# Performance work log

Hardware: AMD Instinct MI355X
Metric: run time of the kernel (lower is better)

Reference implementation:

```python
import jax, jax.numpy as jnp
import numpy as np

N_BASE = 15
SAME_IDS = [[0, 1, 2], [3, 4], [5], [6, 7, 8, 9], [10, 11], [12, 13, 14]]
MEAN_STD = 1.0  # self.mean_std


def setup_inputs() -> dict:
    key = jax.random.key(0)
    batch, channels = 512, 4096
    meta1 = jax.random.normal(key, (batch * N_BASE, channels), dtype=jnp.float32)
    return {"meta1": meta1}


def reference(meta1):
    batch = meta1.shape[0] // N_BASE
    C = meta1.shape[1]
    # [batch, n_base, C] -> [n_base, batch, C]
    m = meta1.reshape(batch, N_BASE, C).transpose(1, 0, 2)
    meta1_mean = m.mean(axis=1)                      # [n_base, C]
    # Original indexes these via .data -> detached; mirror with stop_gradient.
    sub_mean = jax.lax.stop_gradient(meta1_mean.mean(axis=1))          # [n_base]
    sub_std = jax.lax.stop_gradient(jnp.std(meta1_mean, axis=1, ddof=1))  # [n_base], torch std unbiased

    ss_list, mean_list, mean_sum_list = [], [], []
    for line in SAME_IDS:
        idx = jnp.asarray(line)
        g_std = sub_std[idx]
        g_mean = sub_mean[idx]
        if len(line) == 1:
            ss_list.append(g_std[0])          # std_std
            mean_sum_list.append(g_mean[0])   # mean_sum
            mean_list.append(g_mean[0])       # mean
        else:
            ss_list.append(jnp.std(g_std, ddof=1))
            mean_sum_list.append(jnp.std(g_mean, ddof=1))
            mean_list.append(jnp.mean(g_mean))
    ss = jnp.stack(ss_list)        # [G]
    mean = jnp.stack(mean_list)    # [G]
    mean_sum = jnp.stack(mean_sum_list)  # [G]

    G = len(SAME_IDS)
    # subloss[i] = 5e-5 + sum_{j>i} exp((ss_i-ss_j)^2) + mean_std*exp((mean_i-mean_j)^2)
    tri = jnp.triu(jnp.ones((G, G), dtype=bool), k=1)
    pair = jnp.exp((ss[:, None] - ss[None, :]) ** 2) + MEAN_STD * jnp.exp((mean[:, None] - mean[None, :]) ** 2)
    subloss = jnp.float32(5e-5) + jnp.sum(jnp.where(tri, pair, 0.0), axis=1)
    loss = jnp.sum(jnp.log(1.0 + mean_sum / (subloss + mean_sum)))
    return loss
```

## Files before the change

### kernel.cpp

```cpp
#include <hip/hip_runtime.h>

#define NBASE 15
#define CDIM  4096
#define BATCH 512
#define NP    16
#define BPC   (BATCH/NP)

__device__ float  g_partial[NP][NBASE][CDIM];
__device__ double g_stats[2][NBASE];

__global__ __launch_bounds__(256) void k1_partial(const float4* __restrict__ in) {
    const int id = blockIdx.x;
    const int p  = id & 15;
    const int cc = (id >> 4) & 3;
    const int n  = id >> 6;
    const int c4 = cc * 256 + threadIdx.x;
    const int row_f4 = CDIM / 4;

    float4 acc = make_float4(0.f, 0.f, 0.f, 0.f);
    const int b0 = p * BPC;
    #pragma unroll 4
    for (int i = 0; i < BPC; ++i) {
        const int row = (b0 + i) * NBASE + n;
        float4 v = in[(size_t)row * row_f4 + c4];
        acc.x += v.x; acc.y += v.y; acc.z += v.z; acc.w += v.w;
    }
    float4* out4 = reinterpret_cast<float4*>(&g_partial[p][n][0]);
    out4[c4] = acc;
}

__global__ __launch_bounds__(256) void k2_stats() {
    const int n = blockIdx.x;
    double sm = 0.0, sm2 = 0.0;
    for (int c = threadIdx.x; c < CDIM; c += 256) {
        float s = 0.f;
        #pragma unroll
        for (int p = 0; p < NP; ++p) s += g_partial[p][n][c];
        const double m = (double)s * (1.0 / BATCH);
        sm += m; sm2 += m * m;
    }
    __shared__ double red0[256];
    __shared__ double red1[256];
    red0[threadIdx.x] = sm; red1[threadIdx.x] = sm2;
    __syncthreads();
    for (int off = 128; off > 0; off >>= 1) {
        if ((int)threadIdx.x < off) {
            red0[threadIdx.x] += red0[threadIdx.x + off];
            red1[threadIdx.x] += red1[threadIdx.x + off];
        }
        __syncthreads();
    }
    if (threadIdx.x == 0) {
        const double S = red0[0], S2 = red1[0];
        const double mean = S / CDIM;
        const double var  = (S2 - S * S / CDIM) / (CDIM - 1);
        g_stats[0][n] = mean;
        g_stats[1][n] = sqrt(var);
    }
}

__global__ void k3_loss(float* __restrict__ out) {
    if (threadIdx.x != 0 || blockIdx.x != 0) return;
    const int G = 6;
    const int off[G] = {0, 3, 5, 6, 10, 12};
    const int len[G] = {3, 2, 1, 4, 2, 3};
    double ss[G], mn[G], ms[G];
    for (int g = 0; g < G; ++g) {
        const int o = off[g], L = len[g];
        if (L == 1) {
            ss[g] = g_stats[1][o];
            mn[g] = g_stats[0][o];
            ms[g] = g_stats[0][o];
        } else {
            double sm = 0.0, st = 0.0;
            for (int k = 0; k < L; ++k) { sm += g_stats[0][o + k]; st += g_stats[1][o + k]; }
            sm /= L; st /= L;
            double vm = 0.0, vs = 0.0;
            for (int k = 0; k < L; ++k) {
                const double dm = g_stats[0][o + k] - sm; vm += dm * dm;
                const double ds = g_stats[1][o + k] - st; vs += ds * ds;
            }
            mn[g] = sm;
            ms[g] = sqrt(vm / (L - 1));
            ss[g] = sqrt(vs / (L - 1));
        }
    }
    double loss = 0.0;
    for (int i = 0; i < G; ++i) {
        double sl = 5e-5;
        for (int j = i + 1; j < G; ++j) {
            const double ds = ss[i] - ss[j];
            const double dm = mn[i] - mn[j];
            sl += exp(ds * ds) + exp(dm * dm);
        }
        loss += log(1.0 + ms[i] / (sl + ms[i]));
    }
    out[0] = (float)loss;
}

extern "C" void kernel_launch(void* const* d_in, const int* in_sizes, int n_in,
                              void* d_out, int out_size, void* d_ws, size_t ws_size,
                              hipStream_t stream) {
    const float4* in = (const float4*)d_in[0];
    float* out = (float*)d_out;
    hipLaunchKernelGGL(k1_partial, dim3(NBASE * 4 * NP), dim3(256), 0, stream, in);
    hipLaunchKernelGGL(k2_stats,   dim3(NBASE),          dim3(256), 0, stream);
    hipLaunchKernelGGL(k3_loss,    dim3(1),              dim3(64),  0, stream, out);
}
```

Measured before the change: 191.0 us.

## Double batch split, parallelize stats reduction across channel chunks and loss threads

Splits the batch into 32 partial chunks instead of 16, which doubles the k1 grid and fully unrolls its loads. The stats kernel now runs 60 blocks over channel quarters, reading float4 partials, and writes partial sums that the loss kernel combines. The loss kernel spreads the group and pair computations across threads with shared memory. The goal is more parallelism in the memory-bound first stage and in the serial tail kernels, at the cost of a larger partial buffer.

```diff
diff --git a/kernel.cpp b/kernel.cpp
--- a/kernel.cpp
+++ b/kernel.cpp
@@ -2,43 +2,52 @@
 
 #define NBASE 15
 #define CDIM  4096
+#define C4    (CDIM/4)
 #define BATCH 512
-#define NP    16
+#define NP    32
 #define BPC   (BATCH/NP)
 
-__device__ float  g_partial[NP][NBASE][CDIM];
-__device__ double g_stats[2][NBASE];
+__device__ float4 g_partial4[NP][NBASE][C4];
+__device__ double g_red[NBASE][4][2];
+
+__device__ __constant__ int c_pi[15] = {0,0,0,0,0,1,1,1,1,2,2,2,3,3,4};
+__device__ __constant__ int c_pj[15] = {1,2,3,4,5,2,3,4,5,3,4,5,4,5,5};
 
 __global__ __launch_bounds__(256) void k1_partial(const float4* __restrict__ in) {
     const int id = blockIdx.x;
-    const int p  = id & 15;
-    const int cc = (id >> 4) & 3;
-    const int n  = id >> 6;
+    const int p  = id & 31;
+    const int cc = (id >> 5) & 3;
+    const int n  = id >> 7;
     const int c4 = cc * 256 + threadIdx.x;
-    const int row_f4 = CDIM / 4;
 
     float4 acc = make_float4(0.f, 0.f, 0.f, 0.f);
     const int b0 = p * BPC;
-    #pragma unroll 4
+    #pragma unroll
     for (int i = 0; i < BPC; ++i) {
         const int row = (b0 + i) * NBASE + n;
-        float4 v = in[(size_t)row * row_f4 + c4];
+        float4 v = in[(size_t)row * C4 + c4];
         acc.x += v.x; acc.y += v.y; acc.z += v.z; acc.w += v.w;
     }
-    float4* out4 = reinterpret_cast<float4*>(&g_partial[p][n][0]);
-    out4[c4] = acc;
+    g_partial4[p][n][c4] = acc;
 }
 
 __global__ __launch_bounds__(256) void k2_stats() {
-    const int n = blockIdx.x;
-    double sm = 0.0, sm2 = 0.0;
-    for (int c = threadIdx.x; c < CDIM; c += 256) {
-        float s = 0.f;
-        #pragma unroll
-        for (int p = 0; p < NP; ++p) s += g_partial[p][n][c];
-        const double m = (double)s * (1.0 / BATCH);
-        sm += m; sm2 += m * m;
+    const int n  = blockIdx.x >> 2;
+    const int cc = blockIdx.x & 3;
+    const int c4 = cc * 256 + threadIdx.x;
+
+    float4 s = make_float4(0.f, 0.f, 0.f, 0.f);
+    #pragma unroll
+    for (int p = 0; p < NP; ++p) {
+        float4 v = g_partial4[p][n][c4];
+        s.x += v.x; s.y += v.y; s.z += v.z; s.w += v.w;
     }
+    const double inv = 1.0 / BATCH;
+    const double m0 = (double)s.x * inv, m1 = (double)s.y * inv;
+    const double m2 = (double)s.z * inv, m3 = (double)s.w * inv;
+    double sm  = m0 + m1 + m2 + m3;
+    double sm2 = m0*m0 + m1*m1 + m2*m2 + m3*m3;
+
     __shared__ double red0[256];
     __shared__ double red1[256];
     red0[threadIdx.x] = sm; red1[threadIdx.x] = sm2;
@@ -51,51 +60,72 @@
         __syncthreads();
     }
     if (threadIdx.x == 0) {
-        const double S = red0[0], S2 = red1[0];
-        const double mean = S / CDIM;
-        const double var  = (S2 - S * S / CDIM) / (CDIM - 1);
-        g_stats[0][n] = mean;
-        g_stats[1][n] = sqrt(var);
+        g_red[n][cc][0] = red0[0];
+        g_red[n][cc][1] = red1[0];
     }
 }
 
-__global__ void k3_loss(float* __restrict__ out) {
-    if (threadIdx.x != 0 || blockIdx.x != 0) return;
-    const int G = 6;
-    const int off[G] = {0, 3, 5, 6, 10, 12};
-    const int len[G] = {3, 2, 1, 4, 2, 3};
-    double ss[G], mn[G], ms[G];
-    for (int g = 0; g < G; ++g) {
-        const int o = off[g], L = len[g];
+__global__ __launch_bounds__(64) void k3_loss(float* __restrict__ out) {
+    __shared__ double sub_mean[NBASE], sub_std[NBASE];
+    __shared__ double mn[6], ms[6], ssg[6];
+    __shared__ double pairv[15];
+    __shared__ double terms[6];
+    const int t = threadIdx.x;
+
+    if (t < NBASE) {
+        double S = 0.0, S2 = 0.0;
+        #pragma unroll
+        for (int cc = 0; cc < 4; ++cc) { S += g_red[t][cc][0]; S2 += g_red[t][cc][1]; }
+        sub_mean[t] = S / CDIM;
+        sub_std[t]  = sqrt((S2 - S * S / CDIM) / (CDIM - 1));
+    }
+    __syncthreads();
+
+    if (t < 6) {
+        const int off[6] = {0, 3, 5, 6, 10, 12};
+        const int len[6] = {3, 2, 1, 4, 2, 3};
+        const int o = off[t], L = len[t];
         if (L == 1) {
-            ss[g] = g_stats[1][o];
-            mn[g] = g_stats[0][o];
-            ms[g] = g_stats[0][o];
+            ssg[t] = sub_std[o];
+            mn[t]  = sub_mean[o];
+            ms[t]  = sub_mean[o];
         } else {
             double sm = 0.0, st = 0.0;
-            for (int k = 0; k < L; ++k) { sm += g_stats[0][o + k]; st += g_stats[1][o + k]; }
+            for (int k = 0; k < L; ++k) { sm += sub_mean[o + k]; st += sub_std[o + k]; }
             sm /= L; st /= L;
             double vm = 0.0, vs = 0.0;
             for (int k = 0; k < L; ++k) {
-                const double dm = g_stats[0][o + k] - sm; vm += dm * dm;
-                const double ds = g_stats[1][o + k] - st; vs += ds * ds;
+                const double dm = sub_mean[o + k] - sm; vm += dm * dm;
+                const double ds = sub_std[o + k]  - st; vs += ds * ds;
             }
-            mn[g] = sm;
-            ms[g] = sqrt(vm / (L - 1));
-            ss[g] = sqrt(vs / (L - 1));
+            mn[t]  = sm;
+            ms[t]  = sqrt(vm / (L - 1));
+            ssg[t] = sqrt(vs / (L - 1));
         }
     }
-    double loss = 0.0;
-    for (int i = 0; i < G; ++i) {
+    __syncthreads();
+
+    if (t < 15) {
+        const double ds = ssg[c_pi[t]] - ssg[c_pj[t]];
+        const double dm = mn[c_pi[t]]  - mn[c_pj[t]];
+        pairv[t] = exp(ds * ds) + exp(dm * dm);
+    }
+    __syncthreads();
+
+    if (t < 6) {
         double sl = 5e-5;
-        for (int j = i + 1; j < G; ++j) {
-            const double ds = ss[i] - ss[j];
-            const double dm = mn[i] - mn[j];
-            sl += exp(ds * ds) + exp(dm * dm);
-        }
-        loss += log(1.0 + ms[i] / (sl + ms[i]));
+        for (int p = 0; p < 15; ++p)
+            if (c_pi[p] == t) sl += pairv[p];
+        terms[t] = log(1.0 + ms[t] / (sl + ms[t]));
     }
-    out[0] = (float)loss;
+    __syncthreads();
+
+    if (t == 0) {
+        double loss = 0.0;
+        #pragma unroll
+        for (int g = 0; g < 6; ++g) loss += terms[g];
+        out[0] = (float)loss;
+    }
 }
 
 extern "C" void kernel_launch(void* const* d_in, const int* in_sizes, int n_in,
@@ -104,6 +134,6 @@
     const float4* in = (const float4*)d_in[0];
     float* out = (float*)d_out;
     hipLaunchKernelGGL(k1_partial, dim3(NBASE * 4 * NP), dim3(256), 0, stream, in);
-    hipLaunchKernelGGL(k2_stats,   dim3(NBASE),          dim3(256), 0, stream);
+    hipLaunchKernelGGL(k2_stats,   dim3(NBASE * 4),      dim3(256), 0, stream);
     hipLaunchKernelGGL(k3_loss,    dim3(1),              dim3(64),  0, stream, out);
 }
```

New measurement: 185.3 us. 1.03x faster.
